# Performance work log

Measured on AMD Instinct MI355X. Metric: run time of the kernel, lower is better.

The kernel has to match this reference:

```python
import jax, jax.numpy as jnp
import numpy as np

N_HEADS = 12
NEG_INF = -1e9


def rotate_half(x):
    x1, x2 = jnp.split(x, 2, axis=-1)
    return jnp.concatenate((-x2, x1), axis=-1)


def rope_tables(T, D, dtype):
    # matches RotaryEmbedding buffers: emb = cat(freqs, freqs), shape [1,1,T,D]
    inv_freq = 1.0 / (10000.0 ** (jnp.arange(0, D, 2, dtype=jnp.float32) / D))
    t = jnp.arange(T, dtype=jnp.float32)
    freqs = jnp.einsum('i,j->ij', t, inv_freq)
    emb = jnp.concatenate((freqs, freqs), axis=-1)
    return jnp.cos(emb)[None, None].astype(dtype), jnp.sin(emb)[None, None].astype(dtype)


def setup_inputs() -> dict:
    key = jax.random.key(0)
    ks = jax.random.split(key, 5)
    B, T, C = 4, 2048, 768
    s = 1.0 / np.sqrt(C)
    x = jax.random.normal(ks[0], (B, T, C), dtype=jnp.float32)
    wq = jax.random.normal(ks[1], (C, C), dtype=jnp.float32) * s
    wk = jax.random.normal(ks[2], (C, C), dtype=jnp.float32) * s
    wv = jax.random.normal(ks[3], (C, C), dtype=jnp.float32) * s
    wo = jax.random.normal(ks[4], (C, C), dtype=jnp.float32) * s
    causal = jnp.tril(jnp.ones((T, T), dtype=bool))
    mask = jnp.where(causal, 0.0, NEG_INF).astype(jnp.float32)[None, None]
    return {"x": x, "wq": wq, "wk": wk, "wv": wv, "wo": wo, "mask": mask}


def reference(x, wq, wk, wv, wo, mask):
    B, T, C = x.shape
    H = N_HEADS
    D = C // H
    # QKV projections (no bias), reshape to [B,H,T,D]
    def proj(w):
        return (x @ w).reshape(B, T, H, D).transpose(0, 2, 1, 3)
    q, k, v = proj(wq), proj(wk), proj(wv)
    cos, sin = rope_tables(T, D, x.dtype)
    q = q * cos + rotate_half(q) * sin
    k = k * cos + rotate_half(k) * sin
    attn = jnp.einsum('bhqd,bhkd->bhqk', q, k) / jnp.sqrt(jnp.asarray(D, x.dtype))
    attn = attn + mask
    attn = jax.nn.softmax(attn, axis=-1)  # dropout = identity (eval mode)
    out = jnp.einsum('bhqk,bhkd->bhqd', attn, v)
    out = out.transpose(0, 2, 1, 3).reshape(B, T, C)
    return out @ wo
```

## Files before the change

### kernel.cpp

```cpp
#include <hip/hip_runtime.h>
#include <hip/hip_bf16.h>
#include <cmath>

typedef _Float16 f16x8 __attribute__((ext_vector_type(8)));
typedef float f32x4 __attribute__((ext_vector_type(4)));

#define T_SEQ 2048
#define C_DIM 768
#define H_NUM 12
#define NX (8192 * 768)
#define NW (768 * 768)

__device__ __forceinline__ unsigned short f2h(float f) {
    _Float16 h = (_Float16)f;
    return __builtin_bit_cast(unsigned short, h);
}

__device__ __forceinline__ float fexp2(float x) {
#if __has_builtin(__builtin_amdgcn_exp2f)
    return __builtin_amdgcn_exp2f(x);
#else
    return exp2f(x);
#endif
}

__device__ __forceinline__ void gld16(const unsigned short* g, unsigned short* l) {
    __builtin_amdgcn_global_load_lds(
        (const __attribute__((address_space(1))) unsigned int*)g,
        (__attribute__((address_space(3))) unsigned int*)l, 16, 0, 0);
}

__device__ __forceinline__ int ps_idx(int row, int col) {
    return row * 64 + (((col >> 3) ^ (row & 7)) << 3) + (col & 7);
}

__global__ __launch_bounds__(256)
void cast_swz(const float* __restrict__ src, unsigned short* __restrict__ dst) {
    int cidx = blockIdx.x * 256 + threadIdx.x;
    int row = cidx / 96;
    int cp = cidx - row * 96;
    int dchunk = row * 96 + (cp & ~3) + ((cp & 3) ^ (row & 3));
    const float* s = src + (size_t)cidx * 8;
    float4 v0 = *(const float4*)s, v1 = *(const float4*)(s + 4);
    ushort4 a, b;
    a.x = f2h(v0.x); a.y = f2h(v0.y); a.z = f2h(v0.z); a.w = f2h(v0.w);
    b.x = f2h(v1.x); b.y = f2h(v1.y); b.z = f2h(v1.z); b.w = f2h(v1.w);
    unsigned short* d = dst + (size_t)dchunk * 8;
    *(ushort4*)d = a;
    *(ushort4*)(d + 4) = b;
}

__global__ __launch_bounds__(256)
void transpose_cast(const float* __restrict__ w0, const float* __restrict__ w1,
                    const float* __restrict__ w2, const float* __restrict__ w3,
                    unsigned short* __restrict__ dst_base) {
    const float* src = (blockIdx.z == 0) ? w0 : (blockIdx.z == 1) ? w1
                     : (blockIdx.z == 2) ? w2 : w3;
    unsigned short* dst = dst_base + (size_t)blockIdx.z * NW;
    __shared__ float T[64][65];
    const int k0 = blockIdx.x * 64, n0 = blockIdx.y * 64;
    const int tid = threadIdx.x;
    {
        int rowb = tid >> 4, c4 = (tid & 15) * 4;
#pragma unroll
        for (int i = 0; i < 4; ++i) {
            int row = rowb + i * 16;
            float4 v = *(const float4*)&src[(size_t)(k0 + row) * C_DIM + n0 + c4];
            T[row][c4] = v.x; T[row][c4 + 1] = v.y; T[row][c4 + 2] = v.z; T[row][c4 + 3] = v.w;
        }
    }
    __syncthreads();
    {
        int n = tid & 63, kseg = (tid >> 6) * 16;
        int n_glob = n0 + n;
        unsigned short tmp[16];
#pragma unroll
        for (int j = 0; j < 16; ++j) tmp[j] = f2h(T[kseg + j][n]);
        int base = k0 + (kseg & 32);
        int sub = (kseg >> 3) & 3;
        unsigned short* drow = dst + (size_t)n_glob * C_DIM + base;
        *(uint4*)&drow[(sub ^ (n_glob & 3)) << 3]       = *(uint4*)&tmp[0];
        *(uint4*)&drow[((sub + 1) ^ (n_glob & 3)) << 3] = *(uint4*)&tmp[8];
    }
}

__global__ __launch_bounds__(256, 3)
void qkv_gemm(const unsigned short* __restrict__ xb,
              const unsigned short* __restrict__ wt,
              unsigned short* __restrict__ q_ws,
              unsigned short* __restrict__ k_ws,
              unsigned short* __restrict__ vt_ws) {
    const int which = blockIdx.z;
    const unsigned short* W = wt + (size_t)which * NW;
    const int n0 = blockIdx.x * 128, m0 = blockIdx.y * 128;

    __shared__ __align__(16) unsigned short As[2 * 128 * 32];
    __shared__ __align__(16) unsigned short Bs[2 * 128 * 32];

    const int tid = threadIdx.x, lane = tid & 63, w = tid >> 6;
    const int quad = lane >> 4, l16 = lane & 15;
    const int wm = (w >> 1) * 64, wn = (w & 1) * 64;

    f32x4 acc[4][4] = {};

    for (int k0 = 0; k0 < C_DIM; k0 += 64) {
        __syncthreads();
#pragma unroll
        for (int c = 0; c < 4; ++c) {
            int e = c * 256 + tid;
            int p = e >> 9, row = (e >> 2) & 127, ch = e & 3;
            int kc = k0 + p * 32 + ch * 8;
            gld16(xb + (size_t)(m0 + row) * C_DIM + kc, &As[e * 8]);
            gld16(W  + (size_t)(n0 + row) * C_DIM + kc, &Bs[e * 8]);
        }
        __syncthreads();
#pragma unroll
        for (int p = 0; p < 2; ++p) {
            f16x8 af[4], bf[4];
#pragma unroll
            for (int mt = 0; mt < 4; ++mt) {
                int r = wm + mt * 16 + l16;
                af[mt] = *(const f16x8*)&As[p * 4096 + r * 32 + ((quad ^ (r & 3)) << 3)];
            }
#pragma unroll
            for (int nt = 0; nt < 4; ++nt) {
                int r = wn + nt * 16 + l16;
                bf[nt] = *(const f16x8*)&Bs[p * 4096 + r * 32 + ((quad ^ (r & 3)) << 3)];
            }
#pragma unroll
            for (int mt = 0; mt < 4; ++mt)
#pragma unroll
                for (int nt = 0; nt < 4; ++nt)
                    acc[mt][nt] = __builtin_amdgcn_mfma_f32_16x16x32_f16(af[mt], bf[nt], acc[mt][nt], 0, 0, 0);
        }
    }

    const int head = blockIdx.x * 2 + (w & 1);

    if (which < 2) {
        unsigned short* dst = (which == 0) ? q_ws : k_ws;
        const float qscale = 0.18033688011112042f;
#pragma unroll
        for (int ntp = 0; ntp < 2; ++ntp) {
            int d1 = ntp * 16 + l16;
            float invf = __expf(-0.28782313662425572f * (float)d1);
#pragma unroll
            for (int mt = 0; mt < 4; ++mt)
#pragma unroll
                for (int reg = 0; reg < 4; ++reg) {
                    int m = m0 + wm + mt * 16 + quad * 4 + reg;
                    int t = m & (T_SEQ - 1), bb = m >> 11;
                    float sn, cs;
                    __sincosf((float)t * invf, &sn, &cs);
                    float v1 = acc[mt][ntp][reg], v2 = acc[mt][ntp + 2][reg];
                    float o1 = v1 * cs - v2 * sn;
                    float o2 = v2 * cs + v1 * sn;
                    if (which == 0) { o1 *= qscale; o2 *= qscale; }
                    size_t o = ((size_t)(bb * H_NUM + head) * T_SEQ + t) * 64 + d1;
                    dst[o] = f2h(o1);
                    dst[o + 32] = f2h(o2);
                }
        }
    } else {
#pragma unroll
        for (int nt = 0; nt < 4; ++nt) {
            int d = nt * 16 + l16;
#pragma unroll
            for (int mt = 0; mt < 4; ++mt) {
                int m = m0 + wm + mt * 16 + quad * 4;
                int t = m & (T_SEQ - 1), bb = m >> 11;
                ushort4 pk;
                pk.x = f2h(acc[mt][nt][0]); pk.y = f2h(acc[mt][nt][1]);
                pk.z = f2h(acc[mt][nt][2]); pk.w = f2h(acc[mt][nt][3]);
                *(ushort4*)&vt_ws[((size_t)(bb * H_NUM + head) * 64 + d) * T_SEQ + t] = pk;
            }
        }
    }
}

__global__ __launch_bounds__(256, 3)
void flash_attn(const unsigned short* __restrict__ q_ws,
                const unsigned short* __restrict__ k_ws,
                const unsigned short* __restrict__ vt_ws,
                unsigned short* __restrict__ attn_out) {
    __shared__ __align__(16) unsigned short Kbuf[2][64 * 64];
    __shared__ __align__(16) unsigned short Vbuf[2][64 * 64];
    __shared__ __align__(16) unsigned short Ps[4 * 2 * 16 * 64];

    const int pid = blockIdx.x;
    const int xcd = pid & 7, slot = pid >> 3;
    const int bh = xcd * 6 + (slot >> 4);
    const int pr = slot & 15;
    const int qa = pr, qb = 31 - pr;
    const int b = bh / H_NUM, h = bh % H_NUM;

    const int tid = threadIdx.x, lane = tid & 63, w = tid >> 6;
    const int quad = lane >> 4, l16 = lane & 15;
    const size_t base = (size_t)bh * (T_SEQ * 64);

    const unsigned short* qAp = q_ws + base + (size_t)(qa * 64 + w * 16 + l16) * 64 + quad * 8;
    f16x8 aqA0 = *(const f16x8*)(qAp);
    f16x8 aqA1 = *(const f16x8*)(qAp + 32);
    const unsigned short* qBp = q_ws + base + (size_t)(qb * 64 + w * 16 + l16) * 64 + quad * 8;
    f16x8 aqB0 = *(const f16x8*)(qBp);
    f16x8 aqB1 = *(const f16x8*)(qBp + 32);

    f32x4 accA[4] = {}, accB[4] = {};
    float lA[4] = {}, lB[4] = {};
    unsigned short* pbA = Ps + (w * 2 + 0) * 1024;
    unsigned short* pbB = Ps + (w * 2 + 1) * 1024;
    const int swz = l16 & 7;
    const int rd0 = l16 * 64 + ((quad ^ swz) << 3);
    const int rd1 = l16 * 64 + (((quad + 4) ^ swz) << 3);

    const int r_in = lane >> 3;
    const int cpr = lane & 7;
    const int gch = (cpr ^ r_in) * 8;

#define DMA_KV(P, KT)                                                                  \
    {                                                                                  \
        _Pragma("unroll")                                                              \
        for (int j = 0; j < 2; ++j) {                                                  \
            int row = w * 16 + j * 8 + r_in;                                           \
            gld16(k_ws + base + (size_t)((KT) * 64 + row) * 64 + gch,                  \
                  &Kbuf[P][(w * 16 + j * 8) * 64]);                                    \
            gld16(vt_ws + base + (size_t)row * T_SEQ + (KT) * 64 + gch,                \
                  &Vbuf[P][(w * 16 + j * 8) * 64]);                                    \
        }                                                                              \
    }

    const int fo = (quad ^ swz) << 3;

    DMA_KV(0, 0);
    for (int kt = 0; kt <= qb; ++kt) {
        const int cur = kt & 1;
        __syncthreads();
        if (kt < qb) DMA_KV(cur ^ 1, kt + 1);
        const int doA = (kt <= qa);

        f32x4 sB[4] = {}, sA[4] = {};
#pragma unroll
        for (int nt = 0; nt < 4; ++nt) {
            const unsigned short* kr = &Kbuf[cur][(nt * 16 + l16) * 64 + fo];
            f16x8 bk0 = *(const f16x8*)(kr);
            f16x8 bk1 = *(const f16x8*)((const unsigned short*)((size_t)kr ^ 64));
            sB[nt] = __builtin_amdgcn_mfma_f32_16x16x32_f16(aqB0, bk0, sB[nt], 0, 0, 0);
            sB[nt] = __builtin_amdgcn_mfma_f32_16x16x32_f16(aqB1, bk1, sB[nt], 0, 0, 0);
            if (doA) {
                sA[nt] = __builtin_amdgcn_mfma_f32_16x16x32_f16(aqA0, bk0, sA[nt], 0, 0, 0);
                sA[nt] = __builtin_amdgcn_mfma_f32_16x16x32_f16(aqA1, bk1, sA[nt], 0, 0, 0);
            }
        }
        if (kt == qb) {
#pragma unroll
            for (int nt = 0; nt < 4; ++nt)
#pragma unroll
                for (int reg = 0; reg < 4; ++reg)
                    if (nt * 16 + l16 > w * 16 + quad * 4 + reg) sB[nt][reg] = -1e30f;
        }
        if (kt == qa) {
#pragma unroll
            for (int nt = 0; nt < 4; ++nt)
#pragma unroll
                for (int reg = 0; reg < 4; ++reg)
                    if (nt * 16 + l16 > w * 16 + quad * 4 + reg) sA[nt][reg] = -1e30f;
        }

#pragma unroll
        for (int nt = 0; nt < 4; ++nt)
#pragma unroll
            for (int reg = 0; reg < 4; ++reg) {
                float p = fexp2(fminf(sB[nt][reg], 15.0f));
                lB[reg] += p;
                pbB[ps_idx(quad * 4 + reg, nt * 16 + l16)] = f2h(p);
            }
        if (doA) {
#pragma unroll
            for (int nt = 0; nt < 4; ++nt)
#pragma unroll
                for (int reg = 0; reg < 4; ++reg) {
                    float p = fexp2(fminf(sA[nt][reg], 15.0f));
                    lA[reg] += p;
                    pbA[ps_idx(quad * 4 + reg, nt * 16 + l16)] = f2h(p);
                }
        }

        {
            f16x8 apB0 = *(const f16x8*)(pbB + rd0);
            f16x8 apB1 = *(const f16x8*)(pbB + rd1);
#pragma unroll
            for (int nt = 0; nt < 4; ++nt) {
                const unsigned short* vr = &Vbuf[cur][(nt * 16 + l16) * 64 + fo];
                f16x8 bv0 = *(const f16x8*)(vr);
                f16x8 bv1 = *(const f16x8*)((const unsigned short*)((size_t)vr ^ 64));
                accB[nt] = __builtin_amdgcn_mfma_f32_16x16x32_f16(apB0, bv0, accB[nt], 0, 0, 0);
                accB[nt] = __builtin_amdgcn_mfma_f32_16x16x32_f16(apB1, bv1, accB[nt], 0, 0, 0);
            }
        }
        if (doA) {
            f16x8 apA0 = *(const f16x8*)(pbA + rd0);
            f16x8 apA1 = *(const f16x8*)(pbA + rd1);
#pragma unroll
            for (int nt = 0; nt < 4; ++nt) {
                const unsigned short* vr = &Vbuf[cur][(nt * 16 + l16) * 64 + fo];
                f16x8 bv0 = *(const f16x8*)(vr);
                f16x8 bv1 = *(const f16x8*)((const unsigned short*)((size_t)vr ^ 64));
                accA[nt] = __builtin_amdgcn_mfma_f32_16x16x32_f16(apA0, bv0, accA[nt], 0, 0, 0);
                accA[nt] = __builtin_amdgcn_mfma_f32_16x16x32_f16(apA1, bv1, accA[nt], 0, 0, 0);
            }
        }
    }
#undef DMA_KV

#pragma unroll
    for (int reg = 0; reg < 4; ++reg) {
        float v = lB[reg];
        v += __shfl_xor(v, 1); v += __shfl_xor(v, 2);
        v += __shfl_xor(v, 4); v += __shfl_xor(v, 8);
        lB[reg] = 1.0f / v;
        float u = lA[reg];
        u += __shfl_xor(u, 1); u += __shfl_xor(u, 2);
        u += __shfl_xor(u, 4); u += __shfl_xor(u, 8);
        lA[reg] = 1.0f / u;
    }
#pragma unroll
    for (int nt = 0; nt < 4; ++nt)
#pragma unroll
        for (int reg = 0; reg < 4; ++reg) {
            int col = h * 64 + nt * 16 + l16;
            int tB = qb * 64 + w * 16 + quad * 4 + reg;
            attn_out[(size_t)(b * T_SEQ + tB) * C_DIM + col] = f2h(accB[nt][reg] * lB[reg]);
            int tA = qa * 64 + w * 16 + quad * 4 + reg;
            attn_out[(size_t)(b * T_SEQ + tA) * C_DIM + col] = f2h(accA[nt][reg] * lA[reg]);
        }
}

__global__ __launch_bounds__(256, 3)
void out_proj(const unsigned short* __restrict__ ab,
              const unsigned short* __restrict__ wt_o,
              float* __restrict__ out) {
    const int n0 = blockIdx.x * 128, m0 = blockIdx.y * 128;
    __shared__ __align__(16) unsigned short As[2 * 128 * 32];
    __shared__ __align__(16) unsigned short Bs[2 * 128 * 32];

    const int tid = threadIdx.x, lane = tid & 63, w = tid >> 6;
    const int quad = lane >> 4, l16 = lane & 15;
    const int wm = (w >> 1) * 64, wn = (w & 1) * 64;

    f32x4 acc[4][4] = {};
    const int srow = tid >> 1, shalf = tid & 1;

    for (int k0 = 0; k0 < C_DIM; k0 += 64) {
        __syncthreads();
#pragma unroll
        for (int p = 0; p < 2; ++p) {
            const unsigned short* g = ab + (size_t)(m0 + srow) * C_DIM + k0 + p * 32 + shalf * 16;
            uint4 d0 = *(const uint4*)g;
            uint4 d1 = *(const uint4*)(g + 8);
            *(uint4*)&As[p * 4096 + srow * 32 + (((shalf * 2 + 0) ^ (srow & 3)) << 3)] = d0;
            *(uint4*)&As[p * 4096 + srow * 32 + (((shalf * 2 + 1) ^ (srow & 3)) << 3)] = d1;
        }
#pragma unroll
        for (int c = 0; c < 4; ++c) {
            int e = c * 256 + tid;
            int p = e >> 9, row = (e >> 2) & 127, ch = e & 3;
            gld16(wt_o + (size_t)(n0 + row) * C_DIM + k0 + p * 32 + ch * 8, &Bs[e * 8]);
        }
        __syncthreads();
#pragma unroll
        for (int p = 0; p < 2; ++p) {
            f16x8 af[4], bf[4];
#pragma unroll
            for (int mt = 0; mt < 4; ++mt) {
                int r = wm + mt * 16 + l16;
                af[mt] = *(const f16x8*)&As[p * 4096 + r * 32 + ((quad ^ (r & 3)) << 3)];
            }
#pragma unroll
            for (int nt = 0; nt < 4; ++nt) {
                int r = wn + nt * 16 + l16;
                bf[nt] = *(const f16x8*)&Bs[p * 4096 + r * 32 + ((quad ^ (r & 3)) << 3)];
            }
#pragma unroll
            for (int mt = 0; mt < 4; ++mt)
#pragma unroll
                for (int nt = 0; nt < 4; ++nt)
                    acc[mt][nt] = __builtin_amdgcn_mfma_f32_16x16x32_f16(af[mt], bf[nt], acc[mt][nt], 0, 0, 0);
        }
    }

#pragma unroll
    for (int mt = 0; mt < 4; ++mt)
#pragma unroll
        for (int nt = 0; nt < 4; ++nt)
#pragma unroll
            for (int reg = 0; reg < 4; ++reg) {
                int m = m0 + wm + mt * 16 + quad * 4 + reg;
                int n = n0 + wn + nt * 16 + l16;
                out[(size_t)m * C_DIM + n] = acc[mt][nt][reg];
            }
}

extern "C" void kernel_launch(void* const* d_in, const int* in_sizes, int n_in,
                              void* d_out, int out_size, void* d_ws, size_t ws_size,
                              hipStream_t stream) {
    const float* x  = (const float*)d_in[0];
    const float* wq = (const float*)d_in[1];
    const float* wk = (const float*)d_in[2];
    const float* wv = (const float*)d_in[3];
    const float* wo = (const float*)d_in[4];
    float* out = (float*)d_out;

    unsigned short* xb    = (unsigned short*)d_ws;
    unsigned short* wt    = xb + NX;
    unsigned short* q_ws  = wt + 4 * (size_t)NW;
    unsigned short* k_ws  = q_ws + NX;
    unsigned short* vt_ws = k_ws + NX;
    unsigned short* attn  = xb;

    cast_swz<<<NX / 2048, 256, 0, stream>>>(x, xb);
    transpose_cast<<<dim3(12, 12, 4), 256, 0, stream>>>(wq, wk, wv, wo, wt);
    qkv_gemm<<<dim3(6, 64, 3), 256, 0, stream>>>(xb, wt, q_ws, k_ws, vt_ws);
    flash_attn<<<768, 256, 0, stream>>>(q_ws, k_ws, vt_ws, attn);
    out_proj<<<dim3(6, 64), 256, 0, stream>>>(attn, wt + 3 * (size_t)NW, out);
}
```

Measured before the change: 228.8 us.

## Merge prep kernels, XCD-aware GEMM tiling, packed dual P tiles in flash attention

Merges the x cast and the weight transpose into one launch, which removes one kernel launch. Remaps the QKV and output-projection GEMM block indices so each XCD works on a contiguous group of M tiles, improving L2 reuse. In flash attention the two query tiles' probabilities are stored as packed fp16 pairs in one shared buffer and split apart with perm instructions. K/V fragments are loaded into registers once per tile and reused by both query tiles. The cost is higher register pressure from holding the K/V fragments, and the probabilities are now converted with round-toward-zero rather than round-to-nearest.

New measurement: 224.3 us. No clear change (-1.9%).

```diff
diff --git a/kernel.cpp b/kernel.cpp
--- a/kernel.cpp
+++ b/kernel.cpp
@@ -24,63 +24,82 @@
 #endif
 }
 
+__device__ __forceinline__ unsigned int pkrtz(float a, float b) {
+    auto r = __builtin_amdgcn_cvt_pkrtz(a, b);
+    return __builtin_bit_cast(unsigned int, r);
+}
+
+__device__ __forceinline__ unsigned int permlo(unsigned int d0, unsigned int d1) {
+#if __has_builtin(__builtin_amdgcn_perm)
+    return __builtin_amdgcn_perm(d1, d0, 0x05040100u);
+#else
+    return (d0 & 0xffffu) | (d1 << 16);
+#endif
+}
+__device__ __forceinline__ unsigned int permhi(unsigned int d0, unsigned int d1) {
+#if __has_builtin(__builtin_amdgcn_perm)
+    return __builtin_amdgcn_perm(d1, d0, 0x07060302u);
+#else
+    return (d0 >> 16) | (d1 & 0xffff0000u);
+#endif
+}
+
 __device__ __forceinline__ void gld16(const unsigned short* g, unsigned short* l) {
     __builtin_amdgcn_global_load_lds(
         (const __attribute__((address_space(1))) unsigned int*)g,
         (__attribute__((address_space(3))) unsigned int*)l, 16, 0, 0);
 }
 
-__device__ __forceinline__ int ps_idx(int row, int col) {
-    return row * 64 + (((col >> 3) ^ (row & 7)) << 3) + (col & 7);
-}
-
 __global__ __launch_bounds__(256)
-void cast_swz(const float* __restrict__ src, unsigned short* __restrict__ dst) {
-    int cidx = blockIdx.x * 256 + threadIdx.x;
-    int row = cidx / 96;
-    int cp = cidx - row * 96;
-    int dchunk = row * 96 + (cp & ~3) + ((cp & 3) ^ (row & 3));
-    const float* s = src + (size_t)cidx * 8;
-    float4 v0 = *(const float4*)s, v1 = *(const float4*)(s + 4);
-    ushort4 a, b;
-    a.x = f2h(v0.x); a.y = f2h(v0.y); a.z = f2h(v0.z); a.w = f2h(v0.w);
-    b.x = f2h(v1.x); b.y = f2h(v1.y); b.z = f2h(v1.z); b.w = f2h(v1.w);
-    unsigned short* d = dst + (size_t)dchunk * 8;
-    *(ushort4*)d = a;
-    *(ushort4*)(d + 4) = b;
-}
-
-__global__ __launch_bounds__(256)
-void transpose_cast(const float* __restrict__ w0, const float* __restrict__ w1,
-                    const float* __restrict__ w2, const float* __restrict__ w3,
-                    unsigned short* __restrict__ dst_base) {
-    const float* src = (blockIdx.z == 0) ? w0 : (blockIdx.z == 1) ? w1
-                     : (blockIdx.z == 2) ? w2 : w3;
-    unsigned short* dst = dst_base + (size_t)blockIdx.z * NW;
+void prep(const float* __restrict__ x,
+          const float* __restrict__ w0, const float* __restrict__ w1,
+          const float* __restrict__ w2, const float* __restrict__ w3,
+          unsigned short* __restrict__ xb, unsigned short* __restrict__ wt) {
     __shared__ float T[64][65];
-    const int k0 = blockIdx.x * 64, n0 = blockIdx.y * 64;
-    const int tid = threadIdx.x;
-    {
-        int rowb = tid >> 4, c4 = (tid & 15) * 4;
-#pragma unroll
-        for (int i = 0; i < 4; ++i) {
-            int row = rowb + i * 16;
-            float4 v = *(const float4*)&src[(size_t)(k0 + row) * C_DIM + n0 + c4];
-            T[row][c4] = v.x; T[row][c4 + 1] = v.y; T[row][c4 + 2] = v.z; T[row][c4 + 3] = v.w;
-        }
-    }
-    __syncthreads();
-    {
-        int n = tid & 63, kseg = (tid >> 6) * 16;
-        int n_glob = n0 + n;
-        unsigned short tmp[16];
-#pragma unroll
-        for (int j = 0; j < 16; ++j) tmp[j] = f2h(T[kseg + j][n]);
-        int base = k0 + (kseg & 32);
-        int sub = (kseg >> 3) & 3;
-        unsigned short* drow = dst + (size_t)n_glob * C_DIM + base;
-        *(uint4*)&drow[(sub ^ (n_glob & 3)) << 3]       = *(uint4*)&tmp[0];
-        *(uint4*)&drow[((sub + 1) ^ (n_glob & 3)) << 3] = *(uint4*)&tmp[8];
+    const int pid = blockIdx.x;
+    if (pid < 3072) {
+        int cidx = pid * 256 + threadIdx.x;
+        int row = cidx / 96;
+        int cp = cidx - row * 96;
+        int dchunk = row * 96 + (cp & ~3) + ((cp & 3) ^ (row & 3));
+        const float* s = x + (size_t)cidx * 8;
+        float4 v0 = *(const float4*)s, v1 = *(const float4*)(s + 4);
+        ushort4 a, b;
+        a.x = f2h(v0.x); a.y = f2h(v0.y); a.z = f2h(v0.z); a.w = f2h(v0.w);
+        b.x = f2h(v1.x); b.y = f2h(v1.y); b.z = f2h(v1.z); b.w = f2h(v1.w);
+        unsigned short* d = xb + (size_t)dchunk * 8;
+        *(ushort4*)d = a;
+        *(ushort4*)(d + 4) = b;
+    } else {
+        int t = pid - 3072;
+        int z = t / 144, r = t - z * 144;
+        int kx = r / 12, ny = r - kx * 12;
+        const float* src = (z == 0) ? w0 : (z == 1) ? w1 : (z == 2) ? w2 : w3;
+        unsigned short* dst = wt + (size_t)z * NW;
+        const int k0 = kx * 64, n0 = ny * 64;
+        const int tid = threadIdx.x;
+        {
+            int rowb = tid >> 4, c4 = (tid & 15) * 4;
+#pragma unroll
+            for (int i = 0; i < 4; ++i) {
+                int row = rowb + i * 16;
+                float4 v = *(const float4*)&src[(size_t)(k0 + row) * C_DIM + n0 + c4];
+                T[row][c4] = v.x; T[row][c4 + 1] = v.y; T[row][c4 + 2] = v.z; T[row][c4 + 3] = v.w;
+            }
+        }
+        __syncthreads();
+        {
+            int n = tid & 63, kseg = (tid >> 6) * 16;
+            int n_glob = n0 + n;
+            unsigned short tmp[16];
+#pragma unroll
+            for (int j = 0; j < 16; ++j) tmp[j] = f2h(T[kseg + j][n]);
+            int base = k0 + (kseg & 32);
+            int sub = (kseg >> 3) & 3;
+            unsigned short* drow = dst + (size_t)n_glob * C_DIM + base;
+            *(uint4*)&drow[(sub ^ (n_glob & 3)) << 3]       = *(uint4*)&tmp[0];
+            *(uint4*)&drow[((sub + 1) ^ (n_glob & 3)) << 3] = *(uint4*)&tmp[8];
+        }
     }
 }
 
@@ -90,9 +109,12 @@
               unsigned short* __restrict__ q_ws,
               unsigned short* __restrict__ k_ws,
               unsigned short* __restrict__ vt_ws) {
-    const int which = blockIdx.z;
+    const int pid = blockIdx.x;
+    const int xcd = pid & 7, idx = pid >> 3;
+    const int mloc = idx / 18, nw = idx - mloc * 18;
+    const int which = nw % 3, nx = nw / 3;
     const unsigned short* W = wt + (size_t)which * NW;
-    const int n0 = blockIdx.x * 128, m0 = blockIdx.y * 128;
+    const int n0 = nx * 128, m0 = (xcd * 8 + mloc) * 128;
 
     __shared__ __align__(16) unsigned short As[2 * 128 * 32];
     __shared__ __align__(16) unsigned short Bs[2 * 128 * 32];
@@ -135,7 +157,7 @@
         }
     }
 
-    const int head = blockIdx.x * 2 + (w & 1);
+    const int head = nx * 2 + (w & 1);
 
     if (which < 2) {
         unsigned short* dst = (which == 0) ? q_ws : k_ws;
@@ -185,7 +207,7 @@
                 unsigned short* __restrict__ attn_out) {
     __shared__ __align__(16) unsigned short Kbuf[2][64 * 64];
     __shared__ __align__(16) unsigned short Vbuf[2][64 * 64];
-    __shared__ __align__(16) unsigned short Ps[4 * 2 * 16 * 64];
+    __shared__ __align__(16) unsigned int Ps32[4][16 * 64];
 
     const int pid = blockIdx.x;
     const int xcd = pid & 7, slot = pid >> 3;
@@ -207,11 +229,7 @@
 
     f32x4 accA[4] = {}, accB[4] = {};
     float lA[4] = {}, lB[4] = {};
-    unsigned short* pbA = Ps + (w * 2 + 0) * 1024;
-    unsigned short* pbB = Ps + (w * 2 + 1) * 1024;
-    const int swz = l16 & 7;
-    const int rd0 = l16 * 64 + ((quad ^ swz) << 3);
-    const int rd1 = l16 * 64 + (((quad + 4) ^ swz) << 3);
+    unsigned int* pw = &Ps32[w][0];
 
     const int r_in = lane >> 3;
     const int cpr = lane & 7;
@@ -229,7 +247,13 @@
         }                                                                              \
     }
 
-    const int fo = (quad ^ swz) << 3;
+    const int fo = (quad ^ (l16 & 7)) << 3;
+
+    const int rbit = (l16 >> 2) & 1;
+    const int rp0 = l16 * 64 + ((quad * 8 + 16 * rbit) & 63);
+    const int rp1 = l16 * 64 + (((32 + quad * 8) + 16 * rbit) & 63);
+    const int wbase = (quad * 4) * 64;
+    const int wcol0 = ((l16 + 16 * (quad & 1)) & 63);
 
     DMA_KV(0, 0);
     for (int kt = 0; kt <= qb; ++kt) {
@@ -238,17 +262,28 @@
         if (kt < qb) DMA_KV(cur ^ 1, kt + 1);
         const int doA = (kt <= qa);
 
-        f32x4 sB[4] = {}, sA[4] = {};
+        f16x8 bk[4][2], bv[4][2];
 #pragma unroll
         for (int nt = 0; nt < 4; ++nt) {
             const unsigned short* kr = &Kbuf[cur][(nt * 16 + l16) * 64 + fo];
-            f16x8 bk0 = *(const f16x8*)(kr);
-            f16x8 bk1 = *(const f16x8*)((const unsigned short*)((size_t)kr ^ 64));
-            sB[nt] = __builtin_amdgcn_mfma_f32_16x16x32_f16(aqB0, bk0, sB[nt], 0, 0, 0);
-            sB[nt] = __builtin_amdgcn_mfma_f32_16x16x32_f16(aqB1, bk1, sB[nt], 0, 0, 0);
-            if (doA) {
-                sA[nt] = __builtin_amdgcn_mfma_f32_16x16x32_f16(aqA0, bk0, sA[nt], 0, 0, 0);
-                sA[nt] = __builtin_amdgcn_mfma_f32_16x16x32_f16(aqA1, bk1, sA[nt], 0, 0, 0);
+            bk[nt][0] = *(const f16x8*)(kr);
+            bk[nt][1] = *(const f16x8*)((const unsigned short*)((size_t)kr ^ 64));
+            const unsigned short* vr = &Vbuf[cur][(nt * 16 + l16) * 64 + fo];
+            bv[nt][0] = *(const f16x8*)(vr);
+            bv[nt][1] = *(const f16x8*)((const unsigned short*)((size_t)vr ^ 64));
+        }
+
+        f32x4 sB[4] = {}, sA[4] = {};
+#pragma unroll
+        for (int nt = 0; nt < 4; ++nt) {
+            sB[nt] = __builtin_amdgcn_mfma_f32_16x16x32_f16(aqB0, bk[nt][0], sB[nt], 0, 0, 0);
+            sB[nt] = __builtin_amdgcn_mfma_f32_16x16x32_f16(aqB1, bk[nt][1], sB[nt], 0, 0, 0);
+        }
+        if (doA) {
+#pragma unroll
+            for (int nt = 0; nt < 4; ++nt) {
+                sA[nt] = __builtin_amdgcn_mfma_f32_16x16x32_f16(aqA0, bk[nt][0], sA[nt], 0, 0, 0);
+                sA[nt] = __builtin_amdgcn_mfma_f32_16x16x32_f16(aqA1, bk[nt][1], sA[nt], 0, 0, 0);
             }
         }
         if (kt == qb) {
@@ -266,47 +301,51 @@
                     if (nt * 16 + l16 > w * 16 + quad * 4 + reg) sA[nt][reg] = -1e30f;
         }
 
-#pragma unroll
-        for (int nt = 0; nt < 4; ++nt)
-#pragma unroll
-            for (int reg = 0; reg < 4; ++reg) {
-                float p = fexp2(fminf(sB[nt][reg], 15.0f));
-                lB[reg] += p;
-                pbB[ps_idx(quad * 4 + reg, nt * 16 + l16)] = f2h(p);
-            }
         if (doA) {
 #pragma unroll
             for (int nt = 0; nt < 4; ++nt)
 #pragma unroll
                 for (int reg = 0; reg < 4; ++reg) {
-                    float p = fexp2(fminf(sA[nt][reg], 15.0f));
-                    lA[reg] += p;
-                    pbA[ps_idx(quad * 4 + reg, nt * 16 + l16)] = f2h(p);
+                    float pB = fexp2(fminf(sB[nt][reg], 15.0f));
+                    float pA = fexp2(fminf(sA[nt][reg], 15.0f));
+                    lB[reg] += pB;
+                    lA[reg] += pA;
+                    pw[(wbase + reg * 64) + ((wcol0 + nt * 16) & 63)] = pkrtz(pB, pA);
                 }
-        }
-
-        {
-            f16x8 apB0 = *(const f16x8*)(pbB + rd0);
-            f16x8 apB1 = *(const f16x8*)(pbB + rd1);
+        } else {
+#pragma unroll
+            for (int nt = 0; nt < 4; ++nt)
+#pragma unroll
+                for (int reg = 0; reg < 4; ++reg) {
+                    float pB = fexp2(fminf(sB[nt][reg], 15.0f));
+                    lB[reg] += pB;
+                    pw[(wbase + reg * 64) + ((wcol0 + nt * 16) & 63)] = pkrtz(pB, pB);
+                }
+        }
+
+        uint4 c0 = *(const uint4*)(pw + rp0);
+        uint4 c1 = *(const uint4*)(pw + rp0 + 4);
+        uint4 c2 = *(const uint4*)(pw + rp1);
+        uint4 c3 = *(const uint4*)(pw + rp1 + 4);
+
+        uint4 lo0 = { permlo(c0.x, c0.y), permlo(c0.z, c0.w), permlo(c1.x, c1.y), permlo(c1.z, c1.w) };
+        uint4 lo1 = { permlo(c2.x, c2.y), permlo(c2.z, c2.w), permlo(c3.x, c3.y), permlo(c3.z, c3.w) };
+        f16x8 apB0 = __builtin_bit_cast(f16x8, lo0);
+        f16x8 apB1 = __builtin_bit_cast(f16x8, lo1);
+#pragma unroll
+        for (int nt = 0; nt < 4; ++nt) {
+            accB[nt] = __builtin_amdgcn_mfma_f32_16x16x32_f16(apB0, bv[nt][0], accB[nt], 0, 0, 0);
+            accB[nt] = __builtin_amdgcn_mfma_f32_16x16x32_f16(apB1, bv[nt][1], accB[nt], 0, 0, 0);
+        }
+        if (doA) {
+            uint4 hi0 = { permhi(c0.x, c0.y), permhi(c0.z, c0.w), permhi(c1.x, c1.y), permhi(c1.z, c1.w) };
+            uint4 hi1 = { permhi(c2.x, c2.y), permhi(c2.z, c2.w), permhi(c3.x, c3.y), permhi(c3.z, c3.w) };
+            f16x8 apA0 = __builtin_bit_cast(f16x8, hi0);
+            f16x8 apA1 = __builtin_bit_cast(f16x8, hi1);
 #pragma unroll
             for (int nt = 0; nt < 4; ++nt) {
-                const unsigned short* vr = &Vbuf[cur][(nt * 16 + l16) * 64 + fo];
-                f16x8 bv0 = *(const f16x8*)(vr);
-                f16x8 bv1 = *(const f16x8*)((const unsigned short*)((size_t)vr ^ 64));
-                accB[nt] = __builtin_amdgcn_mfma_f32_16x16x32_f16(apB0, bv0, accB[nt], 0, 0, 0);
-                accB[nt] = __builtin_amdgcn_mfma_f32_16x16x32_f16(apB1, bv1, accB[nt], 0, 0, 0);
-            }
-        }
-        if (doA) {
-            f16x8 apA0 = *(const f16x8*)(pbA + rd0);
-            f16x8 apA1 = *(const f16x8*)(pbA + rd1);
-#pragma unroll
-            for (int nt = 0; nt < 4; ++nt) {
-                const unsigned short* vr = &Vbuf[cur][(nt * 16 + l16) * 64 + fo];
-                f16x8 bv0 = *(const f16x8*)(vr);
-                f16x8 bv1 = *(const f16x8*)((const unsigned short*)((size_t)vr ^ 64));
-                accA[nt] = __builtin_amdgcn_mfma_f32_16x16x32_f16(apA0, bv0, accA[nt], 0, 0, 0);
-                accA[nt] = __builtin_amdgcn_mfma_f32_16x16x32_f16(apA1, bv1, accA[nt], 0, 0, 0);
+                accA[nt] = __builtin_amdgcn_mfma_f32_16x16x32_f16(apA0, bv[nt][0], accA[nt], 0, 0, 0);
+                accA[nt] = __builtin_amdgcn_mfma_f32_16x16x32_f16(apA1, bv[nt][1], accA[nt], 0, 0, 0);
             }
         }
     }
@@ -339,7 +378,11 @@
 void out_proj(const unsigned short* __restrict__ ab,
               const unsigned short* __restrict__ wt_o,
               float* __restrict__ out) {
-    const int n0 = blockIdx.x * 128, m0 = blockIdx.y * 128;
+    const int pid = blockIdx.x;
+    const int xcd = pid & 7, idx = pid >> 3;
+    const int mloc = idx / 6, nx = idx - mloc * 6;
+    const int n0 = nx * 128, m0 = (xcd * 8 + mloc) * 128;
+
     __shared__ __align__(16) unsigned short As[2 * 128 * 32];
     __shared__ __align__(16) unsigned short Bs[2 * 128 * 32];
 
@@ -417,9 +460,8 @@
     unsigned short* vt_ws = k_ws + NX;
     unsigned short* attn  = xb;
 
-    cast_swz<<<NX / 2048, 256, 0, stream>>>(x, xb);
-    transpose_cast<<<dim3(12, 12, 4), 256, 0, stream>>>(wq, wk, wv, wo, wt);
-    qkv_gemm<<<dim3(6, 64, 3), 256, 0, stream>>>(xb, wt, q_ws, k_ws, vt_ws);
+    prep<<<3648, 256, 0, stream>>>(x, wq, wk, wv, wo, xb, wt);
+    qkv_gemm<<<1152, 256, 0, stream>>>(xb, wt, q_ws, k_ws, vt_ws);
     flash_attn<<<768, 256, 0, stream>>>(q_ws, k_ws, vt_ws, attn);
-    out_proj<<<dim3(6, 64), 256, 0, stream>>>(attn, wt + 3 * (size_t)NW, out);
-}
+    out_proj<<<384, 256, 0, stream>>>(attn, wt + 3 * (size_t)NW, out);
+}
```
